# Optimization experiments

Hardware: AMD Instinct MI355X
Metric: run time of the kernel (lower is better)

Reference implementation:

```python
import jax, jax.numpy as jnp
import numpy as np
import math

D_MODEL = 256
N_HEADS = 8
NUM_NODES = 20
KSIZE = 3
EPS = 1e-5


def _ln(x, g, b):
    m = jnp.mean(x, axis=-1, keepdims=True)
    v = jnp.mean(jnp.square(x - m), axis=-1, keepdims=True)
    return (x - m) * jax.lax.rsqrt(v + EPS) * g + b


def _conv1d(x_bdn, w_oik):
    # x: [B, D, N], w: [O, I, K], SAME padding, no bias
    return jax.lax.conv_general_dilated(
        x_bdn, w_oik, window_strides=(1,), padding='SAME',
        dimension_numbers=('NCH', 'OIH', 'NCH'))


def setup_inputs() -> dict:
    key = jax.random.key(0)
    ks = jax.random.split(key, 12)
    B, N, D, H, K = 8192, NUM_NODES, D_MODEL, N_HEADS, KSIZE
    s = 1.0 / math.sqrt(D * K)
    inp = {
        'x': jax.random.normal(ks[0], (B, N, D), jnp.float32),
        'wq': jax.random.normal(ks[1], (D, D, K), jnp.float32) * s,
        'wk': jax.random.normal(ks[2], (D, D, K), jnp.float32) * s,
        'wv': jax.random.normal(ks[3], (D, D, K), jnp.float32) * s,
        'gq': jnp.ones((D,), jnp.float32), 'bq': jnp.zeros((D,), jnp.float32),
        'gk': jnp.ones((D,), jnp.float32), 'bk': jnp.zeros((D,), jnp.float32),
        'gv': jnp.ones((D,), jnp.float32), 'bv': jnp.zeros((D,), jnp.float32),
        'rel_table': jax.random.normal(ks[4], (2 * N - 1, H), jnp.float32) * 0.02,
        'gbias': jax.random.normal(ks[5], (H, N, N), jnp.float32) * 0.02,
        'alpha': jnp.float32(1.0),
        'wo': jax.random.normal(ks[6], (D, D), jnp.float32) * (1.0 / math.sqrt(D)),
        'bo': jnp.zeros((D,), jnp.float32),
    }
    return inp


def reference(x, wq, wk, wv, gq, bq, gk, bk, gv, bv, rel_table, gbias, alpha, wo, bo):
    B, N, D = x.shape
    H = N_HEADS
    dk = D // H
    xp = jnp.transpose(x, (0, 2, 1))  # [B, D, N]
    q = x + _ln(jnp.transpose(_conv1d(xp, wq), (0, 2, 1)), gq, bq)
    k = x + _ln(jnp.transpose(_conv1d(xp, wk), (0, 2, 1)), gk, bk)
    v = x + _ln(jnp.transpose(_conv1d(xp, wv), (0, 2, 1)), gv, bv)
    q = q.reshape(B, N, H, dk).transpose(0, 2, 1, 3)  # [B, H, N, dk]
    k = k.reshape(B, N, H, dk).transpose(0, 2, 1, 3)
    v = v.reshape(B, N, H, dk).transpose(0, 2, 1, 3)
    scores = jnp.einsum('bhnd,bhmd->bhnm', q, k) / math.sqrt(dk)
    # relative position bias: index table [2N-1, H] -> [1, H, N, N]
    coords = jnp.arange(N)
    rel_idx = coords[:, None] - coords[None, :] + N - 1  # [N, N]
    rel_bias = rel_table[rel_idx]  # [N, N, H]
    scores = scores + jnp.transpose(rel_bias, (2, 0, 1))[None]
    scores = scores + gbias[None] * alpha
    attn = jax.nn.softmax(scores, axis=-1)
    out = jnp.einsum('bhnm,bhmd->bhnd', attn, v)  # dropout p=0
    out = out.transpose(0, 2, 1, 3).reshape(B, N, D)
    return out @ wo.T + bo
```

## Files before the change

kernel.cpp:

```cpp
#include <hip/hip_runtime.h>
#include <hip/hip_bf16.h>
#include <stdint.h>

#define BATCH 8192
#define NNODE 20
#define MROWS 163840
#define KCONV 768
#define NCONV 768
#define QSCALE 0.17677669529663687f

typedef __bf16 bf16x8 __attribute__((ext_vector_type(8)));
typedef float f32x4 __attribute__((ext_vector_type(4)));
typedef unsigned short u16x8 __attribute__((ext_vector_type(8)));

#define GLOBAL_AS __attribute__((address_space(1)))
#define LDS_AS __attribute__((address_space(3)))

__device__ __forceinline__ void load_lds16(const void* g, void* l) {
  __builtin_amdgcn_global_load_lds((const GLOBAL_AS uint32_t*)g,
                                   (LDS_AS uint32_t*)l, 16, 0, 0);
}

__device__ __forceinline__ float bf2f(unsigned short u) {
  union { unsigned int i; float f; } x;
  x.i = ((unsigned int)u) << 16;
  return x.f;
}

__global__ void prep_kernel(const float* __restrict__ x,
                            const float* __restrict__ wq,
                            const float* __restrict__ wk,
                            const float* __restrict__ wv,
                            const float* __restrict__ wo,
                            __hip_bfloat16* __restrict__ xb,
                            __hip_bfloat16* __restrict__ WcT,
                            __hip_bfloat16* __restrict__ wob,
                            int* __restrict__ zrow) {
  const int stride = gridDim.x * blockDim.x;
  const int gid = blockIdx.x * blockDim.x + threadIdx.x;

  if (gid < 128) zrow[gid] = 0;

  const int n8 = (MROWS * 256) / 8;
  for (int i8 = gid; i8 < n8; i8 += stride) {
    const float4* xp = ((const float4*)x) + (size_t)i8 * 2;
    float4 a = xp[0];
    float4 b = xp[1];
    __align__(16) __hip_bfloat16 h[8];
    h[0] = __float2bfloat16(a.x); h[1] = __float2bfloat16(a.y);
    h[2] = __float2bfloat16(a.z); h[3] = __float2bfloat16(a.w);
    h[4] = __float2bfloat16(b.x); h[5] = __float2bfloat16(b.y);
    h[6] = __float2bfloat16(b.z); h[7] = __float2bfloat16(b.w);
    ((int4*)xb)[i8] = *(const int4*)h;
  }

  for (int idx = gid; idx < NCONV * KCONV; idx += stride) {
    int n = idx / KCONV;
    int j = idx - n * KCONV;
    int c = n >> 8, o = n & 255;
    int t = j >> 8, i = j & 255;
    const float* w = (c == 0) ? wq : (c == 1) ? wk : wv;
    WcT[idx] = __float2bfloat16(w[(o * 256 + i) * 3 + t]);
  }

  for (int idx = gid; idx < 256 * 256; idx += stride) {
    wob[idx] = __float2bfloat16(wo[idx]);
  }
}

__global__ __launch_bounds__(256) void conv_gemm_kernel(
    const __hip_bfloat16* __restrict__ xb,
    const __hip_bfloat16* __restrict__ WcT,
    __hip_bfloat16* __restrict__ y,
    const __hip_bfloat16* __restrict__ zrow) {
  __shared__ __align__(16) __hip_bfloat16 As[128 * 64];
  __shared__ __align__(16) __hip_bfloat16 Bs[128 * 64];

  const int tid = threadIdx.x;
  const int lane = tid & 63;
  const int wave = tid >> 6;
  const int wm = (wave >> 1) << 6;
  const int wn = (wave & 1) << 6;
  const int l16 = lane & 15;
  const int quad = lane >> 4;

  const int bid = blockIdx.x;
  const int xcd = bid & 7;
  const int q = bid >> 3;
  const int qm = q / 6;
  const int nt = q - qm * 6;
  const int m0 = (xcd * 160 + qm) * 128;
  const int n0 = nt * 128;

  const __hip_bfloat16* a_base[4];
  const __hip_bfloat16* z_base[4];
  const __hip_bfloat16* b_base[4];
  int a_node[4];
  int lds_off[4];
#pragma unroll
  for (int it = 0; it < 4; ++it) {
    int flat = ((it * 4 + wave) << 6) + lane;
    int row = flat >> 3;
    int seg = flat & 7;
    int seg_g = seg ^ (row & 7);
    int gr = m0 + row;
    int b = gr / 20;
    int node = gr - b * 20;
    a_node[it] = node;
    a_base[it] = xb + (long)(gr - 1) * 256 + seg_g * 8;
    z_base[it] = zrow + seg_g * 8;
    b_base[it] = WcT + (size_t)(n0 + row) * KCONV + seg_g * 8;
    lds_off[it] = (it * 4 + wave) << 9;
  }

  f32x4 acc[4][4];
  const f32x4 zero = {0.f, 0.f, 0.f, 0.f};
#pragma unroll
  for (int i = 0; i < 4; ++i)
#pragma unroll
    for (int j = 0; j < 4; ++j) acc[i][j] = zero;

  for (int kt = 0; kt < 12; ++kt) {
    const int t = kt >> 2;
    const int i0 = (kt & 3) << 6;
    const int k0 = kt << 6;
#pragma unroll
    for (int it = 0; it < 4; ++it) {
      bool ok = (unsigned)(a_node[it] + t - 1) < 20u;
      const __hip_bfloat16* ga = ok ? (a_base[it] + t * 256 + i0) : z_base[it];
      load_lds16(ga, &As[lds_off[it]]);
      load_lds16(b_base[it] + k0, &Bs[lds_off[it]]);
    }
    __syncthreads();

#pragma unroll
    for (int kk = 0; kk < 64; kk += 32) {
      const int sx = (((kk >> 3) + quad) ^ (l16 & 7)) << 3;
      bf16x8 af[4], bfr[4];
#pragma unroll
      for (int i = 0; i < 4; ++i)
        af[i] = *(const bf16x8*)&As[((wm + i * 16 + l16) << 6) + sx];
#pragma unroll
      for (int j = 0; j < 4; ++j)
        bfr[j] = *(const bf16x8*)&Bs[((wn + j * 16 + l16) << 6) + sx];
#pragma unroll
      for (int i = 0; i < 4; ++i)
#pragma unroll
        for (int j = 0; j < 4; ++j)
          acc[i][j] = __builtin_amdgcn_mfma_f32_16x16x32_bf16(af[i], bfr[j],
                                                              acc[i][j], 0, 0, 0);
    }
    __syncthreads();
  }

#pragma unroll
  for (int i = 0; i < 4; ++i)
#pragma unroll
    for (int j = 0; j < 4; ++j)
#pragma unroll
      for (int r = 0; r < 4; ++r) {
        int row = m0 + wm + i * 16 + quad * 4 + r;
        int col = n0 + wn + j * 16 + l16;
        y[(size_t)row * NCONV + col] = __float2bfloat16(acc[i][j][r]);
      }
}

#define YST 776
__global__ __launch_bounds__(256) void attn5_kernel(
    const __hip_bfloat16* __restrict__ y,
    const __hip_bfloat16* __restrict__ xb,
    const float* __restrict__ rel,
    const float* __restrict__ gbias,
    const float* __restrict__ alpha_p,
    const float* __restrict__ gq, const float* __restrict__ bq,
    const float* __restrict__ gk, const float* __restrict__ bk,
    const float* __restrict__ gv, const float* __restrict__ bv,
    __hip_bfloat16* __restrict__ ao) {
  __shared__ __align__(16) __hip_bfloat16 yS[20 * YST];

  const int b = blockIdx.x;
  const int tid = threadIdx.x;
  const float alpha = alpha_p[0];
  const int lane = tid & 63;
  const int wave = tid >> 6;
  const int l16 = lane & 15;
  const int quad = lane >> 4;
  const f32x4 zero = {0.f, 0.f, 0.f, 0.f};

  const int4* src4 = (const int4*)(y + (size_t)b * NNODE * 768);
#pragma unroll
  for (int p = 0; p < 8; ++p) {
    int idx = tid + p * 256;
    if (idx < 1920) {
      int r = idx / 96;
      int c = idx - r * 96;
      *(int4*)&yS[r * YST + c * 8] = src4[idx];
    }
  }
  u16x8 xr[8];
  if (tid < 240) {
    const int rc = tid >> 2;
    const int p = tid & 3;
    const int r = rc / 3;
    const unsigned short* xp =
        (const unsigned short*)&xb[(((size_t)b * NNODE + r)) << 8];
#pragma unroll
    for (int s = 0; s < 8; ++s) xr[s] = *(const u16x8*)&xp[(s * 4 + p) * 8];
  }
  __syncthreads();

  if (tid < 240) {
    const int rc = tid >> 2;
    const int p = tid & 3;
    const int r = rc / 3;
    const int c = rc - r * 3;
    unsigned short* lp = (unsigned short*)&yS[r * YST + c * 256];

    float sum = 0.f, sq = 0.f;
#pragma unroll
    for (int s = 0; s < 8; ++s) {
      u16x8 v = *(const u16x8*)&lp[(s * 4 + p) * 8];
#pragma unroll
      for (int e = 0; e < 8; ++e) {
        float t = bf2f(v[e]);
        sum += t;
        sq += t * t;
      }
    }
    sum += __shfl_xor(sum, 1, 64); sq += __shfl_xor(sq, 1, 64);
    sum += __shfl_xor(sum, 2, 64); sq += __shfl_xor(sq, 2, 64);

    const float mean = sum * (1.0f / 256.0f);
    const float var = sq * (1.0f / 256.0f) - mean * mean;
    const float rstd = rsqrtf(var + 1e-5f);
    const float osc = (c == 0) ? QSCALE : 1.0f;

    const float* g = (c == 0) ? gq : (c == 1) ? gk : gv;
    const float* bb = (c == 0) ? bq : (c == 1) ? bk : bv;

#pragma unroll
    for (int s = 0; s < 8; ++s) {
      const int c0 = (s * 4 + p) * 8;
      u16x8 v = *(const u16x8*)&lp[c0];
      u16x8 xv = xr[s];
      float4 g0 = *(const float4*)&g[c0];
      float4 g1 = *(const float4*)&g[c0 + 4];
      float4 b0 = *(const float4*)&bb[c0];
      float4 b1 = *(const float4*)&bb[c0 + 4];
      const float* gf0 = (const float*)&g0;
      const float* gf1 = (const float*)&g1;
      const float* bf0 = (const float*)&b0;
      const float* bf1 = (const float*)&b1;
      __align__(16) __hip_bfloat16 h[8];
#pragma unroll
      for (int e = 0; e < 4; ++e)
        h[e] = __float2bfloat16(
            (bf2f(xv[e]) + (bf2f(v[e]) - mean) * rstd * gf0[e] + bf0[e]) * osc);
#pragma unroll
      for (int e = 0; e < 4; ++e)
        h[4 + e] = __float2bfloat16(
            (bf2f(xv[4 + e]) + (bf2f(v[4 + e]) - mean) * rstd * gf1[e] + bf1[e]) * osc);
      *(int4*)&lp[c0] = *(const int4*)h;
    }
  }
  __syncthreads();

  const unsigned short* ySu = (const unsigned short*)yS;
#pragma unroll
  for (int hh = 0; hh < 2; ++hh) {
    const int h = wave * 2 + hh;
    const int rlo = l16;
    const int rhi = (l16 + 16 < 20) ? (l16 + 16) : 19;

    bf16x8 kf0 = *(const bf16x8*)&yS[rlo * YST + 256 + h * 32 + quad * 8];
    bf16x8 kf1 = *(const bf16x8*)&yS[rhi * YST + 256 + h * 32 + quad * 8];
    bf16x8 qf0 = *(const bf16x8*)&yS[rlo * YST + h * 32 + quad * 8];
    bf16x8 qf1 = *(const bf16x8*)&yS[rhi * YST + h * 32 + quad * 8];

    f32x4 c00, c01, c10, c11;
    {
      const float4 g00 = *(const float4*)&gbias[h * 400 + rlo * 20 + quad * 4];
      const float4 g01 = *(const float4*)&gbias[h * 400 + rhi * 20 + quad * 4];
#pragma unroll
      for (int r = 0; r < 4; ++r) {
        const int j0 = quad * 4 + r;
        const int j1 = (16 + j0 < 20) ? (16 + j0) : 19;
        c00[r] = alpha * ((const float*)&g00)[r] + rel[(rlo - j0 + 19) * 8 + h];
        c01[r] = alpha * ((const float*)&g01)[r] + rel[(rhi - j0 + 19) * 8 + h];
        c10[r] = alpha * gbias[h * 400 + rlo * 20 + j1] + rel[(rlo - j1 + 19) * 8 + h];
        c11[r] = alpha * gbias[h * 400 + rhi * 20 + j1] + rel[(rhi - j1 + 19) * 8 + h];
      }
    }
    c00 = __builtin_amdgcn_mfma_f32_16x16x32_bf16(kf0, qf0, c00, 0, 0, 0);
    c01 = __builtin_amdgcn_mfma_f32_16x16x32_bf16(kf0, qf1, c01, 0, 0, 0);
    c10 = __builtin_amdgcn_mfma_f32_16x16x32_bf16(kf1, qf0, c10, 0, 0, 0);
    c11 = __builtin_amdgcn_mfma_f32_16x16x32_bf16(kf1, qf1, c11, 0, 0, 0);

    float p00[4], p10[4], p01[4], p11[4];
    {
      float m = fmaxf(fmaxf(c00[0], c00[1]), fmaxf(c00[2], c00[3]));
      if (quad == 0)
        m = fmaxf(m, fmaxf(fmaxf(c10[0], c10[1]), fmaxf(c10[2], c10[3])));
      m = fmaxf(m, __shfl_xor(m, 16, 64));
      m = fmaxf(m, __shfl_xor(m, 32, 64));
      float s = 0.f;
#pragma unroll
      for (int r = 0; r < 4; ++r) { p00[r] = __expf(c00[r] - m); s += p00[r]; }
#pragma unroll
      for (int r = 0; r < 4; ++r) {
        p10[r] = (quad == 0) ? __expf(c10[r] - m) : 0.f;
        s += p10[r];
      }
      s += __shfl_xor(s, 16, 64);
      s += __shfl_xor(s, 32, 64);
      const float inv = 1.0f / s;
#pragma unroll
      for (int r = 0; r < 4; ++r) { p00[r] *= inv; p10[r] *= inv; }
    }
    {
      float m = fmaxf(fmaxf(c01[0], c01[1]), fmaxf(c01[2], c01[3]));
      if (quad == 0)
        m = fmaxf(m, fmaxf(fmaxf(c11[0], c11[1]), fmaxf(c11[2], c11[3])));
      m = fmaxf(m, __shfl_xor(m, 16, 64));
      m = fmaxf(m, __shfl_xor(m, 32, 64));
      float s = 0.f;
#pragma unroll
      for (int r = 0; r < 4; ++r) { p01[r] = __expf(c01[r] - m); s += p01[r]; }
#pragma unroll
      for (int r = 0; r < 4; ++r) {
        p11[r] = (quad == 0) ? __expf(c11[r] - m) : 0.f;
        s += p11[r];
      }
      s += __shfl_xor(s, 16, 64);
      s += __shfl_xor(s, 32, 64);
      const float inv = 1.0f / s;
#pragma unroll
      for (int r = 0; r < 4; ++r) { p01[r] *= inv; p11[r] *= inv; }
    }

    const int srcA = ((quad * 2) & 3) * 16 + l16;
    const int srcB = ((quad * 2 + 1) & 3) * 16 + l16;
    __align__(16) __hip_bfloat16 aLo[8], aHi[8];
#pragma unroll
    for (int r = 0; r < 4; ++r) {
      float xa = __shfl(p00[r], srcA, 64);
      float xc = __shfl(p00[r], srcB, 64);
      float xt = __shfl(p10[r], l16, 64);
      float lo = (quad < 2) ? xa : ((quad == 2) ? xt : 0.f);
      float hi = (quad < 2) ? xc : 0.f;
      aLo[r] = __float2bfloat16(lo);
      aLo[4 + r] = __float2bfloat16(hi);
      float ya = __shfl(p01[r], srcA, 64);
      float yc = __shfl(p01[r], srcB, 64);
      float yt = __shfl(p11[r], l16, 64);
      lo = (quad < 2) ? ya : ((quad == 2) ? yt : 0.f);
      hi = (quad < 2) ? yc : 0.f;
      aHi[r] = __float2bfloat16(lo);
      aHi[4 + r] = __float2bfloat16(hi);
    }

    __align__(16) __hip_bfloat16 bv0[8], bv1[8];
#pragma unroll
    for (int e = 0; e < 8; ++e) {
      int jj = quad * 8 + e;
      int jc = (jj < 20) ? jj : 19;
      const __hip_bfloat16* vp =
          (const __hip_bfloat16*)&ySu[jc * YST + 512 + h * 32];
      bv0[e] = vp[l16];
      bv1[e] = vp[16 + l16];
    }

    f32x4 d00 = __builtin_amdgcn_mfma_f32_16x16x32_bf16(
        *(const bf16x8*)aLo, *(const bf16x8*)bv0, zero, 0, 0, 0);
    f32x4 d01 = __builtin_amdgcn_mfma_f32_16x16x32_bf16(
        *(const bf16x8*)aLo, *(const bf16x8*)bv1, zero, 0, 0, 0);
    f32x4 d10 = __builtin_amdgcn_mfma_f32_16x16x32_bf16(
        *(const bf16x8*)aHi, *(const bf16x8*)bv0, zero, 0, 0, 0);
    f32x4 d11 = __builtin_amdgcn_mfma_f32_16x16x32_bf16(
        *(const bf16x8*)aHi, *(const bf16x8*)bv1, zero, 0, 0, 0);

    __hip_bfloat16* aob = ao + (((size_t)(b * 20)) << 8) + h * 32;
#pragma unroll
    for (int r = 0; r < 4; ++r) {
      const int i0 = quad * 4 + r;
      aob[i0 * 256 + l16] = __float2bfloat16(d00[r]);
      aob[i0 * 256 + 16 + l16] = __float2bfloat16(d01[r]);
      const int i1 = 16 + i0;
      if (i1 < 20) {
        aob[i1 * 256 + l16] = __float2bfloat16(d10[r]);
        aob[i1 * 256 + 16 + l16] = __float2bfloat16(d11[r]);
      }
    }
  }
}

__global__ __launch_bounds__(256) void proj_gemm_kernel(
    const __hip_bfloat16* __restrict__ ao,
    const __hip_bfloat16* __restrict__ wob,
    const float* __restrict__ bo,
    float* __restrict__ out) {
  __shared__ __align__(16) __hip_bfloat16 As[128 * 64];
  __shared__ __align__(16) __hip_bfloat16 Bs[128 * 64];

  const int tid = threadIdx.x;
  const int lane = tid & 63;
  const int wave = tid >> 6;
  const int wm = (wave >> 1) << 6;
  const int wn = (wave & 1) << 6;
  const int l16 = lane & 15;
  const int quad = lane >> 4;

  const int bid = blockIdx.x;
  const int xcd = bid & 7;
  const int q = bid >> 3;
  const int m0 = (xcd * 160 + (q >> 1)) * 128;
  const int n0 = (q & 1) * 128;

  const __hip_bfloat16* a_base[4];
  const __hip_bfloat16* b_base[4];
  int lds_off[4];
#pragma unroll
  for (int it = 0; it < 4; ++it) {
    int flat = ((it * 4 + wave) << 6) + lane;
    int row = flat >> 3;
    int seg = flat & 7;
    int seg_g = seg ^ (row & 7);
    a_base[it] = ao + (((size_t)(m0 + row)) << 8) + seg_g * 8;
    b_base[it] = wob + (((size_t)(n0 + row)) << 8) + seg_g * 8;
    lds_off[it] = (it * 4 + wave) << 9;
  }

  f32x4 acc[4][4];
  const f32x4 zero = {0.f, 0.f, 0.f, 0.f};
#pragma unroll
  for (int i = 0; i < 4; ++i)
#pragma unroll
    for (int j = 0; j < 4; ++j) acc[i][j] = zero;

  for (int kt = 0; kt < 4; ++kt) {
    const int k0 = kt << 6;
#pragma unroll
    for (int it = 0; it < 4; ++it) {
      load_lds16(a_base[it] + k0, &As[lds_off[it]]);
      load_lds16(b_base[it] + k0, &Bs[lds_off[it]]);
    }
    __syncthreads();

#pragma unroll
    for (int kk = 0; kk < 64; kk += 32) {
      const int sx = (((kk >> 3) + quad) ^ (l16 & 7)) << 3;
      bf16x8 af[4], bfr[4];
#pragma unroll
      for (int i = 0; i < 4; ++i)
        af[i] = *(const bf16x8*)&As[((wm + i * 16 + l16) << 6) + sx];
#pragma unroll
      for (int j = 0; j < 4; ++j)
        bfr[j] = *(const bf16x8*)&Bs[((wn + j * 16 + l16) << 6) + sx];
#pragma unroll
      for (int i = 0; i < 4; ++i)
#pragma unroll
        for (int j = 0; j < 4; ++j)
          acc[i][j] = __builtin_amdgcn_mfma_f32_16x16x32_bf16(af[i], bfr[j],
                                                              acc[i][j], 0, 0, 0);
    }
    __syncthreads();
  }

#pragma unroll
  for (int i = 0; i < 4; ++i)
#pragma unroll
    for (int j = 0; j < 4; ++j) {
      int col = n0 + wn + j * 16 + l16;
      float bias = bo[col];
#pragma unroll
      for (int r = 0; r < 4; ++r) {
        int row = m0 + wm + i * 16 + quad * 4 + r;
        out[(size_t)row * 256 + col] = acc[i][j][r] + bias;
      }
    }
}

extern "C" void kernel_launch(void* const* d_in, const int* in_sizes, int n_in,
                              void* d_out, int out_size, void* d_ws, size_t ws_size,
                              hipStream_t stream) {
  const float* x     = (const float*)d_in[0];
  const float* wq    = (const float*)d_in[1];
  const float* wk    = (const float*)d_in[2];
  const float* wv    = (const float*)d_in[3];
  const float* gq    = (const float*)d_in[4];
  const float* bq    = (const float*)d_in[5];
  const float* gk    = (const float*)d_in[6];
  const float* bk    = (const float*)d_in[7];
  const float* gv    = (const float*)d_in[8];
  const float* bv    = (const float*)d_in[9];
  const float* rel   = (const float*)d_in[10];
  const float* gbias = (const float*)d_in[11];
  const float* alpha = (const float*)d_in[12];
  const float* wo    = (const float*)d_in[13];
  const float* bo    = (const float*)d_in[14];
  float* out = (float*)d_out;

  char* ws = (char*)d_ws;
  __hip_bfloat16* xb  = (__hip_bfloat16*)(ws);
  __hip_bfloat16* y   = (__hip_bfloat16*)(ws + 83886080);
  __hip_bfloat16* ao  = (__hip_bfloat16*)(ws + 335544320);
  __hip_bfloat16* WcT = (__hip_bfloat16*)(ws + 419430400);
  __hip_bfloat16* wob = (__hip_bfloat16*)(ws + 420610048);
  int*            zr  = (int*)(ws + 420741120);

  prep_kernel<<<8192, 256, 0, stream>>>(x, wq, wk, wv, wo, xb, WcT, wob, zr);
  conv_gemm_kernel<<<7680, 256, 0, stream>>>(xb, WcT, y,
                                             (const __hip_bfloat16*)zr);
  attn5_kernel<<<8192, 256, 0, stream>>>(y, xb, rel, gbias, alpha,
                                         gq, bq, gk, bk, gv, bv, ao);
  proj_gemm_kernel<<<2560, 256, 0, stream>>>(ao, wob, bo, out);
}
```

Measured before the change: 820.7 us.

## Triple-buffer conv GEMM with 256x128 tiles and 8-wave blocks

Rewrites the conv GEMM main loop to prefetch two K-tiles ahead into a three-stage LDS ring buffer, replacing the load-sync-compute-sync pattern with vmcnt waits and one barrier per iteration. Block tile grows to 256x128 with 512 threads so each B tile is reused across more rows, and MFMA sections are wrapped in setprio to favour math issue. This is meant to hide global-load latency and cut barrier stalls. The cost is 144KB of LDS per block, which limits occupancy, plus higher register pressure under launch_bounds(512,2).

```diff
diff --git a/kernel.cpp b/kernel.cpp
--- a/kernel.cpp
+++ b/kernel.cpp
@@ -68,49 +68,72 @@
   }
 }
 
-__global__ __launch_bounds__(256) void conv_gemm_kernel(
+__global__ __launch_bounds__(512, 2) void conv_gemm_kernel(
     const __hip_bfloat16* __restrict__ xb,
     const __hip_bfloat16* __restrict__ WcT,
     __hip_bfloat16* __restrict__ y,
     const __hip_bfloat16* __restrict__ zrow) {
-  __shared__ __align__(16) __hip_bfloat16 As[128 * 64];
-  __shared__ __align__(16) __hip_bfloat16 Bs[128 * 64];
+  __shared__ __align__(16) __hip_bfloat16 As[3][256 * 64];
+  __shared__ __align__(16) __hip_bfloat16 Bs[3][128 * 64];
 
   const int tid = threadIdx.x;
   const int lane = tid & 63;
   const int wave = tid >> 6;
-  const int wm = (wave >> 1) << 6;
-  const int wn = (wave & 1) << 6;
+  const int wr = (wave >> 1) << 6;
+  const int wc = (wave & 1) << 6;
   const int l16 = lane & 15;
   const int quad = lane >> 4;
 
   const int bid = blockIdx.x;
   const int xcd = bid & 7;
-  const int q = bid >> 3;
-  const int qm = q / 6;
-  const int nt = q - qm * 6;
-  const int m0 = (xcd * 160 + qm) * 128;
+  const int g = xcd * 480 + (bid >> 3);
+  const int mt = g / 6;
+  const int nt = g - mt * 6;
+  const int m0 = mt * 256;
   const int n0 = nt * 128;
 
   const __hip_bfloat16* a_base[4];
   const __hip_bfloat16* z_base[4];
-  const __hip_bfloat16* b_base[4];
   int a_node[4];
-  int lds_off[4];
+  int a_lds[4];
 #pragma unroll
   for (int it = 0; it < 4; ++it) {
-    int flat = ((it * 4 + wave) << 6) + lane;
+    int flat = tid + it * 512;
     int row = flat >> 3;
     int seg = flat & 7;
     int seg_g = seg ^ (row & 7);
     int gr = m0 + row;
     int b = gr / 20;
-    int node = gr - b * 20;
-    a_node[it] = node;
+    a_node[it] = gr - b * 20;
     a_base[it] = xb + (long)(gr - 1) * 256 + seg_g * 8;
     z_base[it] = zrow + seg_g * 8;
+    a_lds[it] = flat * 8;
+  }
+  const __hip_bfloat16* b_base[2];
+  int b_lds[2];
+#pragma unroll
+  for (int it = 0; it < 2; ++it) {
+    int flat = tid + it * 512;
+    int row = flat >> 3;
+    int seg = flat & 7;
+    int seg_g = seg ^ (row & 7);
     b_base[it] = WcT + (size_t)(n0 + row) * KCONV + seg_g * 8;
-    lds_off[it] = (it * 4 + wave) << 9;
+    b_lds[it] = flat * 8;
+  }
+
+#define STAGE(KT, BUF)                                                        \
+  {                                                                           \
+    const int t_ = (KT) >> 2;                                                 \
+    const int i0_ = ((KT) & 3) << 6;                                          \
+    _Pragma("unroll") for (int it = 0; it < 4; ++it) {                        \
+      bool ok = (unsigned)(a_node[it] + t_ - 1) < 20u;                        \
+      const __hip_bfloat16* ga =                                              \
+          ok ? (a_base[it] + t_ * 256 + i0_) : z_base[it];                    \
+      load_lds16(ga, &As[BUF][a_lds[it]]);                                    \
+    }                                                                         \
+    _Pragma("unroll") for (int it = 0; it < 2; ++it) {                        \
+      load_lds16(b_base[it] + (KT) * 64, &Bs[BUF][b_lds[it]]);                \
+    }                                                                         \
   }
 
   f32x4 acc[4][4];
@@ -120,38 +143,49 @@
 #pragma unroll
     for (int j = 0; j < 4; ++j) acc[i][j] = zero;
 
+  STAGE(0, 0);
+  STAGE(1, 1);
+  asm volatile("s_waitcnt vmcnt(6)" ::: "memory");
+  __builtin_amdgcn_s_barrier();
+  __builtin_amdgcn_sched_barrier(0);
+
+#pragma unroll
   for (int kt = 0; kt < 12; ++kt) {
-    const int t = kt >> 2;
-    const int i0 = (kt & 3) << 6;
-    const int k0 = kt << 6;
-#pragma unroll
-    for (int it = 0; it < 4; ++it) {
-      bool ok = (unsigned)(a_node[it] + t - 1) < 20u;
-      const __hip_bfloat16* ga = ok ? (a_base[it] + t * 256 + i0) : z_base[it];
-      load_lds16(ga, &As[lds_off[it]]);
-      load_lds16(b_base[it] + k0, &Bs[lds_off[it]]);
-    }
-    __syncthreads();
-
+    const int bc = kt % 3;
+    if (kt < 10) {
+      const int bs = (kt + 2) % 3;
+      STAGE(kt + 2, bs);
+    }
 #pragma unroll
     for (int kk = 0; kk < 64; kk += 32) {
       const int sx = (((kk >> 3) + quad) ^ (l16 & 7)) << 3;
       bf16x8 af[4], bfr[4];
 #pragma unroll
       for (int i = 0; i < 4; ++i)
-        af[i] = *(const bf16x8*)&As[((wm + i * 16 + l16) << 6) + sx];
+        af[i] = *(const bf16x8*)&As[bc][((wr + i * 16 + l16) << 6) + sx];
 #pragma unroll
       for (int j = 0; j < 4; ++j)
-        bfr[j] = *(const bf16x8*)&Bs[((wn + j * 16 + l16) << 6) + sx];
+        bfr[j] = *(const bf16x8*)&Bs[bc][((wc + j * 16 + l16) << 6) + sx];
+      __builtin_amdgcn_s_setprio(1);
 #pragma unroll
       for (int i = 0; i < 4; ++i)
 #pragma unroll
         for (int j = 0; j < 4; ++j)
           acc[i][j] = __builtin_amdgcn_mfma_f32_16x16x32_bf16(af[i], bfr[j],
                                                               acc[i][j], 0, 0, 0);
-    }
-    __syncthreads();
-  }
+      __builtin_amdgcn_s_setprio(0);
+    }
+    if (kt < 10) {
+      asm volatile("s_waitcnt vmcnt(6)" ::: "memory");
+    } else if (kt == 10) {
+      asm volatile("s_waitcnt vmcnt(0)" ::: "memory");
+    }
+    if (kt < 11) {
+      __builtin_amdgcn_s_barrier();
+      __builtin_amdgcn_sched_barrier(0);
+    }
+  }
+#undef STAGE
 
 #pragma unroll
   for (int i = 0; i < 4; ++i)
@@ -159,8 +193,8 @@
     for (int j = 0; j < 4; ++j)
 #pragma unroll
       for (int r = 0; r < 4; ++r) {
-        int row = m0 + wm + i * 16 + quad * 4 + r;
-        int col = n0 + wn + j * 16 + l16;
+        int row = m0 + wr + i * 16 + quad * 4 + r;
+        int col = n0 + wc + j * 16 + l16;
         y[(size_t)row * NCONV + col] = __float2bfloat16(acc[i][j][r]);
       }
 }
@@ -509,7 +543,7 @@
   int*            zr  = (int*)(ws + 420741120);
 
   prep_kernel<<<8192, 256, 0, stream>>>(x, wq, wk, wv, wo, xb, WcT, wob, zr);
-  conv_gemm_kernel<<<7680, 256, 0, stream>>>(xb, WcT, y,
+  conv_gemm_kernel<<<3840, 512, 0, stream>>>(xb, WcT, y,
                                              (const __hip_bfloat16*)zr);
   attn5_kernel<<<8192, 256, 0, stream>>>(y, xb, rel, gbias, alpha,
                                          gq, bq, gk, bk, gv, bv, ao);
```

Result: faster. 773.6 us (-5.7%).
